# Performance work log

Measured on AMD Instinct MI355X. Metric: run time of the kernel, lower is better.

The kernel has to match this reference:

```python
import jax, jax.numpy as jnp
import numpy as np

N, E = 50000, 800000
F_IN, F_EDGE = 64, 16
HEADS, C_HEAD = 4, 32
HC = HEADS * C_HEAD  # 128 = hidden_node_channels
MLP_IN = F_IN + HC   # 192
MLP0, MLP1 = 128, 128
NEG_SLOPE = 0.2


def leaky_relu(x):
    return jnp.where(x >= 0, x, NEG_SLOPE * x)


def layer_norm(x, g, b, eps=1e-5):
    mu = jnp.mean(x, axis=-1, keepdims=True)
    var = jnp.mean(jnp.square(x - mu), axis=-1, keepdims=True)
    return (x - mu) * jax.lax.rsqrt(var + eps) * g + b


def setup_inputs() -> dict:
    key = jax.random.key(0)
    ks = jax.random.split(key, 24)
    s = 0.05
    inp = {
        "node_features": jax.random.normal(ks[0], (N, F_IN), jnp.float32),
        "edge_features": jax.random.normal(ks[1], (E, F_EDGE), jnp.float32),
        "edge_index": jax.random.randint(ks[2], (2, E), 0, N, jnp.int32),
        # GATv2Conv params (share_weights=False, bias=True, edge_dim=16)
        "W_l": jax.random.normal(ks[3], (F_IN, HC), jnp.float32) * s,
        "b_l": jax.random.normal(ks[4], (HC,), jnp.float32) * s,
        "W_r": jax.random.normal(ks[5], (F_IN, HC), jnp.float32) * s,
        "b_r": jax.random.normal(ks[6], (HC,), jnp.float32) * s,
        "W_e": jax.random.normal(ks[7], (F_EDGE, HC), jnp.float32) * s,
        "att": jax.random.normal(ks[8], (HEADS, C_HEAD), jnp.float32) * s,
        "gat_bias": jax.random.normal(ks[9], (HC,), jnp.float32) * s,
        # residual_connection: Linear(64->128) + LayerNorm
        "res_W": jax.random.normal(ks[10], (F_IN, MLP1), jnp.float32) * s,
        "res_b": jax.random.normal(ks[11], (MLP1,), jnp.float32) * s,
        "res_g": 1.0 + jax.random.normal(ks[12], (MLP1,), jnp.float32) * s,
        "res_beta": jax.random.normal(ks[13], (MLP1,), jnp.float32) * s,
        # upd MLP: two ffn_blocks (Linear -> LayerNorm -> ReLU)
        "W0": jax.random.normal(ks[14], (MLP_IN, MLP0), jnp.float32) * s,
        "b0": jax.random.normal(ks[15], (MLP0,), jnp.float32) * s,
        "g0": 1.0 + jax.random.normal(ks[16], (MLP0,), jnp.float32) * s,
        "beta0": jax.random.normal(ks[17], (MLP0,), jnp.float32) * s,
        "W1": jax.random.normal(ks[18], (MLP0, MLP1), jnp.float32) * s,
        "b1": jax.random.normal(ks[19], (MLP1,), jnp.float32) * s,
        "g1": 1.0 + jax.random.normal(ks[20], (MLP1,), jnp.float32) * s,
        "beta1": jax.random.normal(ks[21], (MLP1,), jnp.float32) * s,
    }
    return inp


def reference(node_features, edge_features, edge_index,
              W_l, b_l, W_r, b_r, W_e, att, gat_bias,
              res_W, res_b, res_g, res_beta,
              W0, b0, g0, beta0, W1, b1, g1, beta1):
    src, dst = edge_index[0], edge_index[1]

    # ---- GATv2Conv ----
    x_l = (node_features @ W_l + b_l).reshape(N, HEADS, C_HEAD)  # source transform
    x_r = (node_features @ W_r + b_r).reshape(N, HEADS, C_HEAD)  # target transform
    e = (edge_features @ W_e).reshape(E, HEADS, C_HEAD)

    x_j = x_l[src]                      # [E,H,C] messages
    m = x_j + x_r[dst] + e              # [E,H,C]
    logits = jnp.sum(leaky_relu(m) * att, axis=-1)  # [E,H]

    # segment softmax over incoming edges of each destination node
    mx = jax.ops.segment_max(logits, dst, num_segments=N)      # [N,H]
    ex = jnp.exp(logits - mx[dst])                             # [E,H]
    den = jax.ops.segment_sum(ex, dst, num_segments=N)         # [N,H]
    alpha = ex / den[dst]                                      # [E,H]

    agg = jax.ops.segment_sum(alpha[..., None] * x_j, dst, num_segments=N)
    gat_out = agg.reshape(N, HC) + gat_bias                    # [N,128]

    # ---- residual concat-MLP ----
    identity = layer_norm(node_features @ res_W + res_b, res_g, res_beta)
    h = jnp.concatenate([node_features, gat_out], axis=-1)     # [N,192]
    h = jax.nn.relu(layer_norm(h @ W0 + b0, g0, beta0))
    h = jax.nn.relu(layer_norm(h @ W1 + b1, g1, beta1))
    return identity + h
```

## Files before the change

kernel.cpp:

```cpp
#include <hip/hip_runtime.h>

#define NN 50000
#define NE 800000
#define NB 196
#define K1B 782

typedef __attribute__((ext_vector_type(8))) short bf16x8;
typedef __attribute__((ext_vector_type(4))) float f32x4;
typedef __attribute__((ext_vector_type(2))) _Float16 h2f;

__device__ __forceinline__ int rfl(int v) { return __builtin_amdgcn_readfirstlane(v); }

__device__ __forceinline__ unsigned short bfb(float x) {
    union { float f; unsigned u; } v; v.f = x;
    unsigned r = v.u + 0x7FFFu + ((v.u >> 16) & 1u);
    return (unsigned short)(r >> 16);
}
__device__ __forceinline__ unsigned pkbf(float lo, float hi) {
    return ((unsigned)bfb(hi) << 16) | (unsigned)bfb(lo);
}
__device__ __forceinline__ unsigned pkh2(float a, float b) {
    union { h2f h; unsigned u; } x;
    x.h.x = (_Float16)a; x.h.y = (_Float16)b;
    return x.u;
}
__device__ __forceinline__ float fdot2u(unsigned a, unsigned b, float c) {
    union { unsigned u; h2f h; } ua, ub; ua.u = a; ub.u = b;
    return __builtin_amdgcn_fdot2(ua.h, ub.h, c, false);
}

__device__ __forceinline__ float dpp_reduce16(float p) {
    int t;
    t = __builtin_amdgcn_update_dpp(0, __float_as_int(p), 0xB1, 0xF, 0xF, false);
    p += __int_as_float(t);
    t = __builtin_amdgcn_update_dpp(0, __float_as_int(p), 0x4E, 0xF, 0xF, false);
    p += __int_as_float(t);
    t = __builtin_amdgcn_update_dpp(0, __float_as_int(p), 0x124, 0xF, 0xF, false);
    p += __int_as_float(t);
    t = __builtin_amdgcn_update_dpp(0, __float_as_int(p), 0x128, 0xF, 0xF, false);
    p += __int_as_float(t);
    return p;
}

__global__ __launch_bounds__(256) void k0_prep(
    const float* __restrict__ W_l, const float* __restrict__ W_r,
    const float* __restrict__ res_W, const float* __restrict__ W0,
    const float* __restrict__ W1, const float* __restrict__ W_e,
    const float* __restrict__ ef,
    unsigned short* __restrict__ Wtl, unsigned short* __restrict__ Wtr,
    unsigned short* __restrict__ Wtres, unsigned short* __restrict__ Wt0,
    unsigned short* __restrict__ Wt1,
    unsigned* __restrict__ Wep, unsigned* __restrict__ efp,
    int* __restrict__ deg, int* __restrict__ row_start)
{
    const int t0 = blockIdx.x * 256 + threadIdx.x;
    const int nth = gridDim.x * 256;
    for (int t = t0; t < NE * 8; t += nth) {
        float2 v = *(const float2*)(ef + 2 * t);
        efp[t] = pkh2(v.x, v.y);
    }
    if (t0 < 24576) { int n = t0 / 192, k = t0 - n * 192; Wt0[t0] = bfb(W0[k * 128 + n]); }
    if (t0 < 16384) { int n = t0 >> 7, k = t0 & 127; Wt1[t0] = bfb(W1[k * 128 + n]); }
    if (t0 < 8192) {
        int n = t0 >> 6, k = t0 & 63;
        Wtl[t0]   = bfb(W_l[k * 128 + n]);
        Wtr[t0]   = bfb(W_r[k * 128 + n]);
        Wtres[t0] = bfb(res_W[k * 128 + n]);
    }
    if (t0 < 1024) {
        int c = t0 >> 3, j = t0 & 7;
        Wep[t0] = pkh2(W_e[(2 * j) * 128 + c], W_e[(2 * j + 1) * 128 + c]);
    }
    if (t0 < NN) deg[t0] = 0;
    if (t0 == 0) row_start[NN] = NE;
}

__global__ __launch_bounds__(256, 4) void ka_nodes_degree(
    const float* __restrict__ nf,
    const unsigned short* __restrict__ Wtl, const float* __restrict__ b_l,
    const unsigned short* __restrict__ Wtr, const float* __restrict__ b_r,
    const unsigned short* __restrict__ Wtres, const float* __restrict__ res_b,
    const float* __restrict__ res_g, const float* __restrict__ res_beta,
    float* __restrict__ x_l, float* __restrict__ x_r, float* __restrict__ ident,
    const int* __restrict__ eidx, int* __restrict__ deg)
{
    if (blockIdx.x >= K1B) {
        int e = (blockIdx.x - K1B) * 256 + threadIdx.x;
        if (e < NE) atomicAdd(deg + eidx[NE + e], 1);
        return;
    }
    __shared__ __align__(16) unsigned As32[64 * 36];
    const int tid = threadIdx.x;
    const int node0 = blockIdx.x * 64;

    for (int i = tid; i < 64 * 32; i += 256) {
        int n = i >> 5, c2 = i & 31;
        int gn = node0 + n;
        float2 v = make_float2(0.f, 0.f);
        if (gn < NN) v = *(const float2*)(nf + gn * 64 + 2 * c2);
        As32[n * 36 + c2] = pkbf(v.x, v.y);
    }
    __syncthreads();

    const int lane = tid & 63, w = tid >> 6;
    const int c = lane & 15, ko = lane >> 4;
    const unsigned short* As = (const unsigned short*)As32;
    bf16x8 a0 = *(const bf16x8*)(As + (w * 16 + c) * 72 + 0 * 32 + ko * 8);
    bf16x8 a1 = *(const bf16x8*)(As + (w * 16 + c) * 72 + 1 * 32 + ko * 8);
    const int lrow0 = node0 + w * 16 + 4 * ko;

    #pragma unroll
    for (int p = 0; p < 3; ++p) {
        const unsigned short* Wt = (p == 0) ? Wtl : (p == 1) ? Wtr : Wtres;
        f32x4 acc[8];
        #pragma unroll
        for (int nt = 0; nt < 8; ++nt) acc[nt] = f32x4{0.f, 0.f, 0.f, 0.f};
        #pragma unroll
        for (int nt = 0; nt < 8; ++nt) {
            bf16x8 bf0 = *(const bf16x8*)(Wt + (nt * 16 + c) * 64 + 0 * 32 + ko * 8);
            acc[nt] = __builtin_amdgcn_mfma_f32_16x16x32_bf16(a0, bf0, acc[nt], 0, 0, 0);
            bf16x8 bf1 = *(const bf16x8*)(Wt + (nt * 16 + c) * 64 + 1 * 32 + ko * 8);
            acc[nt] = __builtin_amdgcn_mfma_f32_16x16x32_bf16(a1, bf1, acc[nt], 0, 0, 0);
        }
        if (p < 2) {
            const float* bias = (p == 0) ? b_l : b_r;
            float* o = (p == 0) ? x_l : x_r;
            float bv[8];
            #pragma unroll
            for (int nt = 0; nt < 8; ++nt) bv[nt] = bias[nt * 16 + c];
            #pragma unroll
            for (int reg = 0; reg < 4; ++reg) {
                int row = lrow0 + reg;
                if (row < NN) {
                    #pragma unroll
                    for (int nt = 0; nt < 8; ++nt)
                        o[row * 128 + nt * 16 + c] = acc[nt][reg] + bv[nt];
                }
            }
        } else {
            float bv[8], gv[8], tv[8];
            #pragma unroll
            for (int nt = 0; nt < 8; ++nt) {
                bv[nt] = res_b[nt * 16 + c];
                gv[nt] = res_g[nt * 16 + c];
                tv[nt] = res_beta[nt * 16 + c];
            }
            #pragma unroll
            for (int reg = 0; reg < 4; ++reg) {
                float sum = 0.f, sq = 0.f, hv[8];
                #pragma unroll
                for (int nt = 0; nt < 8; ++nt) {
                    float v = acc[nt][reg] + bv[nt];
                    hv[nt] = v; sum += v; sq += v * v;
                }
                #pragma unroll
                for (int m = 1; m <= 8; m <<= 1) {
                    sum += __shfl_xor(sum, m, 64);
                    sq  += __shfl_xor(sq, m, 64);
                }
                float mean = sum * (1.f / 128.f);
                float inv  = rsqrtf(sq * (1.f / 128.f) - mean * mean + 1e-5f);
                int row = lrow0 + reg;
                if (row < NN) {
                    #pragma unroll
                    for (int nt = 0; nt < 8; ++nt)
                        ident[row * 128 + nt * 16 + c] =
                            (hv[nt] - mean) * inv * gv[nt] + tv[nt];
                }
            }
        }
    }
}

__global__ __launch_bounds__(256) void k3a_blocksum(
    const int* __restrict__ deg, int* __restrict__ bsum)
{
    __shared__ int ws[4];
    int i = blockIdx.x * 256 + threadIdx.x;
    int v = (i < NN) ? deg[i] : 0;
    #pragma unroll
    for (int m = 32; m >= 1; m >>= 1) v += __shfl_xor(v, m, 64);
    if ((threadIdx.x & 63) == 0) ws[threadIdx.x >> 6] = v;
    __syncthreads();
    if (threadIdx.x == 0) bsum[blockIdx.x] = ws[0] + ws[1] + ws[2] + ws[3];
}

__global__ __launch_bounds__(256) void k3c_apply(
    const int* __restrict__ deg, const int* __restrict__ bsum,
    int* __restrict__ row_start, int* __restrict__ cursor)
{
    __shared__ int wsum[4];
    __shared__ int roff[4];
    const int tid = threadIdx.x, lane = tid & 63, wid = tid >> 6;
    int bv = (tid < blockIdx.x) ? bsum[tid] : 0;
    #pragma unroll
    for (int m = 32; m >= 1; m >>= 1) bv += __shfl_xor(bv, m, 64);
    if (lane == 0) roff[wid] = bv;

    int i = blockIdx.x * 256 + tid;
    int v = (i < NN) ? deg[i] : 0;
    int sc = v;
    #pragma unroll
    for (int m = 1; m < 64; m <<= 1) {
        int t = __shfl_up(sc, m, 64);
        if (lane >= m) sc += t;
    }
    if (lane == 63) wsum[wid] = sc;
    __syncthreads();
    int off = roff[0] + roff[1] + roff[2] + roff[3];
    for (int w = 0; w < wid; ++w) off += wsum[w];
    int excl = off + sc - v;
    if (i < NN) { row_start[i] = excl; cursor[i] = excl; }
}

__global__ __launch_bounds__(256) void k4_scatter(
    const int* __restrict__ eidx, int* __restrict__ cursor,
    int2* __restrict__ csr_es)
{
    int e = blockIdx.x * 256 + threadIdx.x;
    if (e >= NE) return;
    int dst = eidx[NE + e];
    int srcn = eidx[e];
    int pos = atomicAdd(cursor + dst, 1);
    csr_es[pos] = make_int2(e, srcn);
}

__global__ __launch_bounds__(256, 4) void k5_attn_aggregate(
    const int2* __restrict__ csr_es, const int* __restrict__ row_start,
    const unsigned* __restrict__ efp, const unsigned* __restrict__ Wep,
    const float* __restrict__ att,
    const float* __restrict__ x_l, const float* __restrict__ x_r,
    const float* __restrict__ gat_bias,
    float* __restrict__ gat_out)
{
    const int lane = threadIdx.x & 63;
    const int node = (blockIdx.x * 256 + threadIdx.x) >> 6;
    if (node >= NN) return;
    const int c = lane * 2;

    uint4 t0 = *(const uint4*)(Wep + c * 8);
    uint4 t1 = *(const uint4*)(Wep + c * 8 + 4);
    uint4 t2 = *(const uint4*)(Wep + (c + 1) * 8);
    uint4 t3 = *(const uint4*)(Wep + (c + 1) * 8 + 4);
    unsigned wx0 = t0.x, wx1 = t0.y, wx2 = t0.z, wx3 = t0.w;
    unsigned wx4 = t1.x, wx5 = t1.y, wx6 = t1.z, wx7 = t1.w;
    unsigned wy0 = t2.x, wy1 = t2.y, wy2 = t2.z, wy3 = t2.w;
    unsigned wy4 = t3.x, wy5 = t3.y, wy6 = t3.z, wy7 = t3.w;

    const float2 a2 = *(const float2*)(att + c);
    const float2 xr = *(const float2*)(x_r + node * 128 + c);
    const uint4* __restrict__ efq = (const uint4*)efp;
    const float2* __restrict__ xlc = (const float2*)(x_l + c);

    const int sj  = rfl(row_start[node]);
    const int epj = rfl(row_start[node + 1]);

    float den = 0.f, n0 = 0.f, n1 = 0.f;

    if (sj < epj) {
        int2 es0 = csr_es[sj];
        int eid = rfl(es0.x), src = rfl(es0.y);
        uint4 E0 = efq[eid * 2 + 0], E1 = efq[eid * 2 + 1];
        float2 X = xlc[src * 64];

        for (int j = sj; j < epj; ++j) {
            asm volatile("" : "+v"(wx0), "+v"(wx1), "+v"(wx2), "+v"(wx3),
                              "+v"(wx4), "+v"(wx5), "+v"(wx6), "+v"(wx7));
            asm volatile("" : "+v"(wy0), "+v"(wy1), "+v"(wy2), "+v"(wy3),
                              "+v"(wy4), "+v"(wy5), "+v"(wy6), "+v"(wy7));
            uint4 cE0 = E0, cE1 = E1;
            float2 cX = X;
            if (j + 1 < epj) {
                int2 es = csr_es[j + 1];
                int e1 = rfl(es.x), s1 = rfl(es.y);
                E0 = efq[e1 * 2 + 0]; E1 = efq[e1 * 2 + 1];
                X = xlc[s1 * 64];
            }
            float ax = cX.x + xr.x;
            float bx = 0.f;
            float ay = cX.y + xr.y;
            float by = 0.f;
            ax = fdot2u(cE0.x, wx0, ax);  ay = fdot2u(cE0.x, wy0, ay);
            bx = fdot2u(cE0.y, wx1, bx);  by = fdot2u(cE0.y, wy1, by);
            ax = fdot2u(cE0.z, wx2, ax);  ay = fdot2u(cE0.z, wy2, ay);
            bx = fdot2u(cE0.w, wx3, bx);  by = fdot2u(cE0.w, wy3, by);
            ax = fdot2u(cE1.x, wx4, ax);  ay = fdot2u(cE1.x, wy4, ay);
            bx = fdot2u(cE1.y, wx5, bx);  by = fdot2u(cE1.y, wy5, by);
            ax = fdot2u(cE1.z, wx6, ax);  ay = fdot2u(cE1.z, wy6, ay);
            bx = fdot2u(cE1.w, wx7, bx);  by = fdot2u(cE1.w, wy7, by);
            float evx = ax + bx;
            float evy = ay + by;

            float lx = fmaxf(evx, 0.2f * evx);
            float ly = fmaxf(evy, 0.2f * evy);
            float p = lx * a2.x + ly * a2.y;
            p = dpp_reduce16(p);
            float ev = __expf(p);
            den += ev;
            n0 += ev * cX.x;
            n1 += ev * cX.y;
        }
    }
    float rden = (den > 0.f) ? (1.f / den) : 0.f;
    float2 gb = *(const float2*)(gat_bias + c);
    float2 o; o.x = n0 * rden + gb.x; o.y = n1 * rden + gb.y;
    *(float2*)(gat_out + node * 128 + c) = o;
}

__global__ __launch_bounds__(256, 4) void k6_mlp_mfma(
    const float* __restrict__ nf, const float* __restrict__ gat,
    const float* __restrict__ ident,
    const unsigned short* __restrict__ Wt0, const float* __restrict__ b0,
    const float* __restrict__ g0, const float* __restrict__ be0,
    const unsigned short* __restrict__ Wt1, const float* __restrict__ b1,
    const float* __restrict__ g1, const float* __restrict__ be1,
    float* __restrict__ out)
{
    __shared__ __align__(16) unsigned LDS[64 * 100];
    const int tid = threadIdx.x;
    const int node0 = blockIdx.x * 64;

    for (int i = tid; i < 64 * 96; i += 256) {
        int n = i / 96, c2 = i - n * 96;
        int gn = node0 + n;
        float2 v = make_float2(0.f, 0.f);
        if (gn < NN)
            v = (c2 < 32) ? *(const float2*)(nf + gn * 64 + 2 * c2)
                          : *(const float2*)(gat + gn * 128 + 2 * (c2 - 32));
        LDS[n * 100 + c2] = pkbf(v.x, v.y);
    }
    __syncthreads();

    const int lane = tid & 63, w = tid >> 6;
    const int c = lane & 15, ko = lane >> 4;
    const int lrow = w * 16 + 4 * ko;

    f32x4 acc[8];
    #pragma unroll
    for (int nt = 0; nt < 8; ++nt) acc[nt] = f32x4{0.f, 0.f, 0.f, 0.f};

    #pragma unroll
    for (int kb = 0; kb < 6; ++kb) {
        bf16x8 a = *(const bf16x8*)((const unsigned short*)LDS +
                                    (w * 16 + c) * 200 + kb * 32 + ko * 8);
        #pragma unroll
        for (int nt = 0; nt < 8; ++nt) {
            bf16x8 b = *(const bf16x8*)(Wt0 + (nt * 16 + c) * 192 + kb * 32 + ko * 8);
            acc[nt] = __builtin_amdgcn_mfma_f32_16x16x32_bf16(a, b, acc[nt], 0, 0, 0);
        }
    }

    float bv[8], gv[8], tv[8];
    #pragma unroll
    for (int nt = 0; nt < 8; ++nt) {
        bv[nt] = b0[nt * 16 + c];
        gv[nt] = g0[nt * 16 + c];
        tv[nt] = be0[nt * 16 + c];
    }
    __syncthreads();

    unsigned short* Hs = (unsigned short*)LDS;
    #pragma unroll
    for (int reg = 0; reg < 4; ++reg) {
        float sum = 0.f, sq = 0.f, hv[8];
        #pragma unroll
        for (int nt = 0; nt < 8; ++nt) {
            float v = acc[nt][reg] + bv[nt];
            hv[nt] = v; sum += v; sq += v * v;
        }
        #pragma unroll
        for (int m = 1; m <= 8; m <<= 1) {
            sum += __shfl_xor(sum, m, 64);
            sq  += __shfl_xor(sq, m, 64);
        }
        float mean = sum * (1.f / 128.f);
        float inv  = rsqrtf(sq * (1.f / 128.f) - mean * mean + 1e-5f);
        #pragma unroll
        for (int nt = 0; nt < 8; ++nt) {
            float h = fmaxf((hv[nt] - mean) * inv * gv[nt] + tv[nt], 0.f);
            Hs[(lrow + reg) * 136 + nt * 16 + c] = bfb(h);
        }
    }
    __syncthreads();

    #pragma unroll
    for (int nt = 0; nt < 8; ++nt) acc[nt] = f32x4{0.f, 0.f, 0.f, 0.f};
    #pragma unroll
    for (int kb = 0; kb < 4; ++kb) {
        bf16x8 a = *(const bf16x8*)((const unsigned short*)LDS +
                                    (w * 16 + c) * 136 + kb * 32 + ko * 8);
        #pragma unroll
        for (int nt = 0; nt < 8; ++nt) {
            bf16x8 b = *(const bf16x8*)(Wt1 + (nt * 16 + c) * 128 + kb * 32 + ko * 8);
            acc[nt] = __builtin_amdgcn_mfma_f32_16x16x32_bf16(a, b, acc[nt], 0, 0, 0);
        }
    }

    #pragma unroll
    for (int nt = 0; nt < 8; ++nt) {
        bv[nt] = b1[nt * 16 + c];
        gv[nt] = g1[nt * 16 + c];
        tv[nt] = be1[nt * 16 + c];
    }
    #pragma unroll
    for (int reg = 0; reg < 4; ++reg) {
        float sum = 0.f, sq = 0.f, hv[8];
        #pragma unroll
        for (int nt = 0; nt < 8; ++nt) {
            float v = acc[nt][reg] + bv[nt];
            hv[nt] = v; sum += v; sq += v * v;
        }
        #pragma unroll
        for (int m = 1; m <= 8; m <<= 1) {
            sum += __shfl_xor(sum, m, 64);
            sq  += __shfl_xor(sq, m, 64);
        }
        float mean = sum * (1.f / 128.f);
        float inv  = rsqrtf(sq * (1.f / 128.f) - mean * mean + 1e-5f);
        int row = node0 + lrow + reg;
        if (row < NN) {
            #pragma unroll
            for (int nt = 0; nt < 8; ++nt) {
                float h = fmaxf((hv[nt] - mean) * inv * gv[nt] + tv[nt], 0.f);
                int col = nt * 16 + c;
                out[row * 128 + col] = ident[row * 128 + col] + h;
            }
        }
    }
}

extern "C" void kernel_launch(void* const* d_in, const int* in_sizes, int n_in,
                              void* d_out, int out_size, void* d_ws, size_t ws_size,
                              hipStream_t stream)
{
    const float* nf       = (const float*)d_in[0];
    const float* ef       = (const float*)d_in[1];
    const int*   eidx     = (const int*)d_in[2];
    const float* W_l      = (const float*)d_in[3];
    const float* b_l      = (const float*)d_in[4];
    const float* W_r      = (const float*)d_in[5];
    const float* b_r      = (const float*)d_in[6];
    const float* W_e      = (const float*)d_in[7];
    const float* att      = (const float*)d_in[8];
    const float* gat_bias = (const float*)d_in[9];
    const float* res_W    = (const float*)d_in[10];
    const float* res_b    = (const float*)d_in[11];
    const float* res_g    = (const float*)d_in[12];
    const float* res_beta = (const float*)d_in[13];
    const float* W0       = (const float*)d_in[14];
    const float* b0       = (const float*)d_in[15];
    const float* g0       = (const float*)d_in[16];
    const float* beta0    = (const float*)d_in[17];
    const float* W1       = (const float*)d_in[18];
    const float* b1       = (const float*)d_in[19];
    const float* g1       = (const float*)d_in[20];
    const float* beta1    = (const float*)d_in[21];
    float* out = (float*)d_out;

    char* ws = (char*)d_ws;
    size_t off = 0;
    auto alloc = [&](size_t bytes) -> void* {
        void* p = ws + off;
        off += (bytes + 255) & ~(size_t)255;
        return p;
    };
    float* x_l     = (float*)alloc((size_t)NN * 128 * 4);
    float* x_r     = (float*)alloc((size_t)NN * 128 * 4);
    float* ident   = (float*)alloc((size_t)NN * 128 * 4);
    int* deg       = (int*)alloc((size_t)NN * 4);
    int* row_start = (int*)alloc((size_t)(NN + 1) * 4);
    int* cursor    = (int*)alloc((size_t)NN * 4);
    int* bsum      = (int*)alloc((size_t)(NB + 1) * 4);
    int2* csr_es   = (int2*)alloc((size_t)NE * 8);
    float* gat_out = (float*)alloc((size_t)NN * 128 * 4);
    unsigned short* Wtl   = (unsigned short*)alloc(8192 * 2);
    unsigned short* Wtr   = (unsigned short*)alloc(8192 * 2);
    unsigned short* Wtres = (unsigned short*)alloc(8192 * 2);
    unsigned short* Wt0   = (unsigned short*)alloc(24576 * 2);
    unsigned short* Wt1   = (unsigned short*)alloc(16384 * 2);
    unsigned* Wep = (unsigned*)alloc(1024 * 4);
    unsigned* efp = (unsigned*)alloc((size_t)NE * 8 * 4);

    k0_prep<<<8192, 256, 0, stream>>>(W_l, W_r, res_W, W0, W1, W_e, ef,
                                      Wtl, Wtr, Wtres, Wt0, Wt1, Wep, efp,
                                      deg, row_start);

    ka_nodes_degree<<<K1B + (NE + 255) / 256, 256, 0, stream>>>(
        nf, Wtl, b_l, Wtr, b_r, Wtres, res_b, res_g, res_beta,
        x_l, x_r, ident, eidx, deg);

    k3a_blocksum<<<NB, 256, 0, stream>>>(deg, bsum);
    k3c_apply<<<NB, 256, 0, stream>>>(deg, bsum, row_start, cursor);

    k4_scatter<<<(NE + 255) / 256, 256, 0, stream>>>(eidx, cursor, csr_es);

    k5_attn_aggregate<<<(NN * 64 + 255) / 256, 256, 0, stream>>>(
        csr_es, row_start, efp, Wep, att, x_l, x_r, gat_bias, gat_out);

    k6_mlp_mfma<<<(NN + 63) / 64, 256, 0, stream>>>(
        nf, gat_out, ident, Wt0, b0, g0, beta0, Wt1, b1, g1, beta1, out);
}
```

Measured before the change: 400.6 us.

## Store x_l as fp16, reuse degree atomics for CSR rank, deepen gather prefetch

The source-node transform x_l is now stored as packed fp16 pairs, which halves the bytes gathered per edge in the attention kernel. The degree-counting atomic records each edge's rank, so the scatter kernel places edges at row_start+rank without a second atomic pass and the cursor array goes away. The attention loop is unrolled three ways with a two-deep software prefetch, meant to hide the latency of the gathered loads. The cost is lower precision on the messages (fp16 instead of fp32) and an extra rank array of one int per edge.

```diff
diff --git a/kernel.cpp b/kernel.cpp
--- a/kernel.cpp
+++ b/kernel.cpp
@@ -81,12 +81,12 @@
     const unsigned short* __restrict__ Wtr, const float* __restrict__ b_r,
     const unsigned short* __restrict__ Wtres, const float* __restrict__ res_b,
     const float* __restrict__ res_g, const float* __restrict__ res_beta,
-    float* __restrict__ x_l, float* __restrict__ x_r, float* __restrict__ ident,
-    const int* __restrict__ eidx, int* __restrict__ deg)
+    unsigned* __restrict__ xlp, float* __restrict__ x_r, float* __restrict__ ident,
+    const int* __restrict__ eidx, int* __restrict__ deg, int* __restrict__ rank)
 {
     if (blockIdx.x >= K1B) {
         int e = (blockIdx.x - K1B) * 256 + threadIdx.x;
-        if (e < NE) atomicAdd(deg + eidx[NE + e], 1);
+        if (e < NE) rank[e] = atomicAdd(deg + eidx[NE + e], 1);
         return;
     }
     __shared__ __align__(16) unsigned As32[64 * 36];
@@ -122,19 +122,32 @@
             bf16x8 bf1 = *(const bf16x8*)(Wt + (nt * 16 + c) * 64 + 1 * 32 + ko * 8);
             acc[nt] = __builtin_amdgcn_mfma_f32_16x16x32_bf16(a1, bf1, acc[nt], 0, 0, 0);
         }
-        if (p < 2) {
-            const float* bias = (p == 0) ? b_l : b_r;
-            float* o = (p == 0) ? x_l : x_r;
+        if (p == 0) {
             float bv[8];
             #pragma unroll
-            for (int nt = 0; nt < 8; ++nt) bv[nt] = bias[nt * 16 + c];
+            for (int nt = 0; nt < 8; ++nt) bv[nt] = b_l[nt * 16 + c];
+            #pragma unroll
+            for (int reg = 0; reg < 4; ++reg) {
+                int row = lrow0 + reg;
+                #pragma unroll
+                for (int nt = 0; nt < 8; ++nt) {
+                    float v = acc[nt][reg] + bv[nt];
+                    float v2 = __shfl_xor(v, 1, 64);
+                    if (row < NN && (lane & 1) == 0)
+                        xlp[row * 64 + nt * 8 + (c >> 1)] = pkh2(v, v2);
+                }
+            }
+        } else if (p == 1) {
+            float bv[8];
+            #pragma unroll
+            for (int nt = 0; nt < 8; ++nt) bv[nt] = b_r[nt * 16 + c];
             #pragma unroll
             for (int reg = 0; reg < 4; ++reg) {
                 int row = lrow0 + reg;
                 if (row < NN) {
                     #pragma unroll
                     for (int nt = 0; nt < 8; ++nt)
-                        o[row * 128 + nt * 16 + c] = acc[nt][reg] + bv[nt];
+                        x_r[row * 128 + nt * 16 + c] = acc[nt][reg] + bv[nt];
                 }
             }
         } else {
@@ -187,7 +200,7 @@
 
 __global__ __launch_bounds__(256) void k3c_apply(
     const int* __restrict__ deg, const int* __restrict__ bsum,
-    int* __restrict__ row_start, int* __restrict__ cursor)
+    int* __restrict__ row_start)
 {
     __shared__ int wsum[4];
     __shared__ int roff[4];
@@ -210,26 +223,24 @@
     int off = roff[0] + roff[1] + roff[2] + roff[3];
     for (int w = 0; w < wid; ++w) off += wsum[w];
     int excl = off + sc - v;
-    if (i < NN) { row_start[i] = excl; cursor[i] = excl; }
+    if (i < NN) row_start[i] = excl;
 }
 
 __global__ __launch_bounds__(256) void k4_scatter(
-    const int* __restrict__ eidx, int* __restrict__ cursor,
-    int2* __restrict__ csr_es)
+    const int* __restrict__ eidx, const int* __restrict__ row_start,
+    const int* __restrict__ rank, int2* __restrict__ csr_es)
 {
     int e = blockIdx.x * 256 + threadIdx.x;
     if (e >= NE) return;
     int dst = eidx[NE + e];
-    int srcn = eidx[e];
-    int pos = atomicAdd(cursor + dst, 1);
-    csr_es[pos] = make_int2(e, srcn);
+    csr_es[row_start[dst] + rank[e]] = make_int2(e, eidx[e]);
 }
 
 __global__ __launch_bounds__(256, 4) void k5_attn_aggregate(
     const int2* __restrict__ csr_es, const int* __restrict__ row_start,
     const unsigned* __restrict__ efp, const unsigned* __restrict__ Wep,
     const float* __restrict__ att,
-    const float* __restrict__ x_l, const float* __restrict__ x_r,
+    const unsigned* __restrict__ xlp, const float* __restrict__ x_r,
     const float* __restrict__ gat_bias,
     float* __restrict__ gat_out)
 {
@@ -250,7 +261,7 @@
     const float2 a2 = *(const float2*)(att + c);
     const float2 xr = *(const float2*)(x_r + node * 128 + c);
     const uint4* __restrict__ efq = (const uint4*)efp;
-    const float2* __restrict__ xlc = (const float2*)(x_l + c);
+    const unsigned* __restrict__ xlc = xlp + lane;
 
     const int sj  = rfl(row_start[node]);
     const int epj = rfl(row_start[node + 1]);
@@ -258,48 +269,60 @@
     float den = 0.f, n0 = 0.f, n1 = 0.f;
 
     if (sj < epj) {
-        int2 es0 = csr_es[sj];
-        int eid = rfl(es0.x), src = rfl(es0.y);
-        uint4 E0 = efq[eid * 2 + 0], E1 = efq[eid * 2 + 1];
-        float2 X = xlc[src * 64];
-
-        for (int j = sj; j < epj; ++j) {
-            asm volatile("" : "+v"(wx0), "+v"(wx1), "+v"(wx2), "+v"(wx3),
-                              "+v"(wx4), "+v"(wx5), "+v"(wx6), "+v"(wx7));
-            asm volatile("" : "+v"(wy0), "+v"(wy1), "+v"(wy2), "+v"(wy3),
-                              "+v"(wy4), "+v"(wy5), "+v"(wy6), "+v"(wy7));
-            uint4 cE0 = E0, cE1 = E1;
-            float2 cX = X;
-            if (j + 1 < epj) {
-                int2 es = csr_es[j + 1];
-                int e1 = rfl(es.x), s1 = rfl(es.y);
-                E0 = efq[e1 * 2 + 0]; E1 = efq[e1 * 2 + 1];
-                X = xlc[s1 * 64];
-            }
-            float ax = cX.x + xr.x;
-            float bx = 0.f;
-            float ay = cX.y + xr.y;
-            float by = 0.f;
-            ax = fdot2u(cE0.x, wx0, ax);  ay = fdot2u(cE0.x, wy0, ay);
-            bx = fdot2u(cE0.y, wx1, bx);  by = fdot2u(cE0.y, wy1, by);
-            ax = fdot2u(cE0.z, wx2, ax);  ay = fdot2u(cE0.z, wy2, ay);
-            bx = fdot2u(cE0.w, wx3, bx);  by = fdot2u(cE0.w, wy3, by);
-            ax = fdot2u(cE1.x, wx4, ax);  ay = fdot2u(cE1.x, wy4, ay);
-            bx = fdot2u(cE1.y, wx5, bx);  by = fdot2u(cE1.y, wy5, by);
-            ax = fdot2u(cE1.z, wx6, ax);  ay = fdot2u(cE1.z, wy6, ay);
-            bx = fdot2u(cE1.w, wx7, bx);  by = fdot2u(cE1.w, wy7, by);
-            float evx = ax + bx;
-            float evy = ay + by;
-
-            float lx = fmaxf(evx, 0.2f * evx);
-            float ly = fmaxf(evy, 0.2f * evy);
-            float p = lx * a2.x + ly * a2.y;
-            p = dpp_reduce16(p);
-            float ev = __expf(p);
-            den += ev;
-            n0 += ev * cX.x;
-            n1 += ev * cX.y;
-        }
+        const int last = epj - 1;
+        uint4 aE0, aE1, bE0, bE1, cE0, cE1;
+        unsigned aX, bX, cX;
+
+#define LOADS(E0_, E1_, X_, IDX_)                                          \
+        { int jc = (IDX_); if (jc > last) jc = last;                       \
+          int2 es = csr_es[jc];                                            \
+          int eid = rfl(es.x), srcn = rfl(es.y);                           \
+          E0_ = efq[eid * 2 + 0]; E1_ = efq[eid * 2 + 1];                  \
+          X_  = xlc[srcn * 64]; }
+
+#define CONSUME(E0_, E1_, X_)                                              \
+        { asm volatile("" : "+v"(wx0), "+v"(wx1), "+v"(wx2), "+v"(wx3),    \
+                            "+v"(wx4), "+v"(wx5), "+v"(wx6), "+v"(wx7));   \
+          asm volatile("" : "+v"(wy0), "+v"(wy1), "+v"(wy2), "+v"(wy3),    \
+                            "+v"(wy4), "+v"(wy5), "+v"(wy6), "+v"(wy7));   \
+          union { unsigned u; h2f h; } ux; ux.u = (X_);                    \
+          float cx0 = (float)ux.h.x, cx1 = (float)ux.h.y;                  \
+          float ax = cx0 + xr.x;                                           \
+          float ay = cx1 + xr.y;                                           \
+          float bx = 0.f, by = 0.f;                                        \
+          ax = fdot2u((E0_).x, wx0, ax);  ay = fdot2u((E0_).x, wy0, ay);   \
+          bx = fdot2u((E0_).y, wx1, bx);  by = fdot2u((E0_).y, wy1, by);   \
+          ax = fdot2u((E0_).z, wx2, ax);  ay = fdot2u((E0_).z, wy2, ay);   \
+          bx = fdot2u((E0_).w, wx3, bx);  by = fdot2u((E0_).w, wy3, by);   \
+          ax = fdot2u((E1_).x, wx4, ax);  ay = fdot2u((E1_).x, wy4, ay);   \
+          bx = fdot2u((E1_).y, wx5, bx);  by = fdot2u((E1_).y, wy5, by);   \
+          ax = fdot2u((E1_).z, wx6, ax);  ay = fdot2u((E1_).z, wy6, ay);   \
+          bx = fdot2u((E1_).w, wx7, bx);  by = fdot2u((E1_).w, wy7, by);   \
+          float evx = ax + bx;                                             \
+          float evy = ay + by;                                             \
+          float lx = fmaxf(evx, 0.2f * evx);                               \
+          float ly = fmaxf(evy, 0.2f * evy);                               \
+          float p = lx * a2.x + ly * a2.y;                                 \
+          p = dpp_reduce16(p);                                             \
+          float ev = __expf(p);                                            \
+          den += ev; n0 += ev * cx0; n1 += ev * cx1; }
+
+        LOADS(aE0, aE1, aX, sj);
+        LOADS(bE0, bE1, bX, sj + 1);
+        int j = sj;
+        while (j + 3 <= epj) {
+            LOADS(cE0, cE1, cX, j + 2);
+            CONSUME(aE0, aE1, aX);
+            LOADS(aE0, aE1, aX, j + 3);
+            CONSUME(bE0, bE1, bX);
+            LOADS(bE0, bE1, bX, j + 4);
+            CONSUME(cE0, cE1, cX);
+            j += 3;
+        }
+        if (j < epj)     CONSUME(aE0, aE1, aX);
+        if (j + 1 < epj) CONSUME(bE0, bE1, bX);
+#undef LOADS
+#undef CONSUME
     }
     float rden = (den > 0.f) ? (1.f / den) : 0.f;
     float2 gb = *(const float2*)(gat_bias + c);
@@ -464,12 +487,12 @@
         off += (bytes + 255) & ~(size_t)255;
         return p;
     };
-    float* x_l     = (float*)alloc((size_t)NN * 128 * 4);
+    unsigned* xlp  = (unsigned*)alloc((size_t)NN * 64 * 4);
     float* x_r     = (float*)alloc((size_t)NN * 128 * 4);
     float* ident   = (float*)alloc((size_t)NN * 128 * 4);
     int* deg       = (int*)alloc((size_t)NN * 4);
     int* row_start = (int*)alloc((size_t)(NN + 1) * 4);
-    int* cursor    = (int*)alloc((size_t)NN * 4);
+    int* rank      = (int*)alloc((size_t)NE * 4);
     int* bsum      = (int*)alloc((size_t)(NB + 1) * 4);
     int2* csr_es   = (int2*)alloc((size_t)NE * 8);
     float* gat_out = (float*)alloc((size_t)NN * 128 * 4);
@@ -487,15 +510,15 @@
 
     ka_nodes_degree<<<K1B + (NE + 255) / 256, 256, 0, stream>>>(
         nf, Wtl, b_l, Wtr, b_r, Wtres, res_b, res_g, res_beta,
-        x_l, x_r, ident, eidx, deg);
+        xlp, x_r, ident, eidx, deg, rank);
 
     k3a_blocksum<<<NB, 256, 0, stream>>>(deg, bsum);
-    k3c_apply<<<NB, 256, 0, stream>>>(deg, bsum, row_start, cursor);
-
-    k4_scatter<<<(NE + 255) / 256, 256, 0, stream>>>(eidx, cursor, csr_es);
+    k3c_apply<<<NB, 256, 0, stream>>>(deg, bsum, row_start);
+
+    k4_scatter<<<(NE + 255) / 256, 256, 0, stream>>>(eidx, row_start, rank, csr_es);
 
     k5_attn_aggregate<<<(NN * 64 + 255) / 256, 256, 0, stream>>>(
-        csr_es, row_start, efp, Wep, att, x_l, x_r, gat_bias, gat_out);
+        csr_es, row_start, efp, Wep, att, xlp, x_r, gat_bias, gat_out);
 
     k6_mlp_mfma<<<(NN + 63) / 64, 256, 0, stream>>>(
         nf, gat_out, ident, Wt0, b0, g0, beta0, Wt1, b1, g1, beta1, out);
```

Result: faster. 342.2 us (-14.6%).
